# Optimization experiments

Measured on AMD Instinct MI355X. Metric: run time of the kernel, lower is better.

The kernel has to match this reference:

```python
import jax, jax.numpy as jnp
import numpy as np
from jax import lax

B, T = 8192, 4096


def setup_inputs() -> dict:
    key = jax.random.key(0)
    ks = jax.random.split(key, 16)
    P = jax.random.uniform(ks[0], (B, T, 1), dtype=jnp.float32) * 10.0  # precipitation, mm
    lengths = jax.random.randint(ks[1], (B,), 1, T + 1, dtype=jnp.int32)
    initial_S = jax.random.uniform(ks[2], (4,), dtype=jnp.float32) * 20.0  # initial tank levels
    Area = jnp.array([100.0], dtype=jnp.float32)  # catchment area km^2
    baseflow = jnp.array([0.0], dtype=jnp.float32)  # unused by forward, kept for signature fidelity

    def u(k, lo, hi):
        return jax.random.uniform(k, (1,), dtype=jnp.float32) * (hi - lo) + lo

    params = {
        "outflow_rate_1_h1": u(ks[3], 0.05, 0.25),
        "outflow_rate_1_h2": u(ks[4], 0.05, 0.10),
        "height_1_h1": u(ks[5], 40.0, 60.0),
        "height_1_h2": u(ks[6], 0.0, 40.0),
        "inflow_rate_2": u(ks[7], 0.01, 0.30),
        "outflow_rate_2": u(ks[8], 0.005, 0.30),
        "height_2": u(ks[9], 0.0, 30.0),
        "inflow_rate_3": u(ks[10], 0.005, 0.20),
        "outflow_rate_3": u(ks[11], 0.005, 0.15),
        "height_3": u(ks[12], 0.0, 30.0),
        "inflow_rate_4": u(ks[13], 0.005, 0.10),
        "outflow_rate_4": u(ks[14], 0.0006, 0.10),
    }
    return {"P": P, "lengths": lengths, "initial_S": initial_S, "Area": Area,
            "baseflow": baseflow, **params}


def reference(P, lengths, initial_S, Area, baseflow,
              outflow_rate_1_h1, outflow_rate_1_h2, height_1_h1, height_1_h2,
              inflow_rate_2, outflow_rate_2, height_2,
              inflow_rate_3, outflow_rate_3, height_3,
              inflow_rate_4, outflow_rate_4):
    Pq = P[..., 0]                              # [B, T]
    b, t = Pq.shape
    # valid_mask[b, t] = (lengths[b] > t), as in pad_packed_sequence masking
    mask = (jnp.arange(t)[None, :] < lengths[:, None]).astype(Pq.dtype)  # [B, T]
    w_init = tuple(jnp.broadcast_to(initial_S[i], (b,)) for i in range(4))

    def step(carry, xs):
        w1, w2, w3, w4 = carry
        p, m = xs                               # [B] each
        # Tank 1: two side outlets + bottom percolation into tank 2
        of1h1 = jnp.maximum(outflow_rate_1_h1 * (w1 - height_1_h1 + p), 0.0) * m
        of1h2 = jnp.maximum(outflow_rate_1_h2 * (w1 - height_1_h2 + p), 0.0) * m
        of1 = (of1h1 + of1h2) * m
        out12 = jnp.maximum(inflow_rate_2 * (w1 + p), 0.0) * m
        w1 = w1 + (p - of1 - out12) * m
        # Tank 2
        of2 = jnp.maximum(outflow_rate_2 * (w2 + out12 - height_2), 0.0) * m
        out23 = jnp.maximum(inflow_rate_3 * (w2 + out12), 0.0) * m
        w2 = w2 + (out12 - of2 - out23) * m
        # Tank 3
        of3 = jnp.maximum(outflow_rate_3 * (w3 + out23 - height_3), 0.0) * m
        out34 = jnp.maximum(inflow_rate_4 * (w3 + out23), 0.0) * m
        w3 = w3 + (out23 - of3 - out34) * m
        # Tank 4 (deep baseflow tank)
        of4 = jnp.maximum(outflow_rate_4 * (w4 + out34), 0.0) * m
        w4 = w4 + (out34 - of4) * m
        total = (of1 + of2 + of3 + of4) * m
        return (w1, w2, w3, w4), total * Area / 3.6   # mm -> m^3/s conversion

    _, ys = lax.scan(step, w_init, (Pq.T, mask.T))    # ys: [T, B]
    return ys.T                                        # [B, T]
```

## Files before the change

kernel.cpp:

```cpp
#include <hip/hip_runtime.h>
#include <stdint.h>


__device__ __forceinline__ float quad_rot1(float x) {
    int xi = __builtin_bit_cast(int, x);
    int r = __builtin_amdgcn_update_dpp(xi, xi, 0x93, 0xF, 0xF, false);
    return __builtin_bit_cast(float, r);
}

__device__ __forceinline__ float quad_bcast(float x, int s) {
    int xi = __builtin_bit_cast(int, x);
    int r;
    switch (s & 3) {
    case 0:  r = __builtin_amdgcn_update_dpp(xi, xi, 0x00, 0xF, 0xF, false); break;
    case 1:  r = __builtin_amdgcn_update_dpp(xi, xi, 0x55, 0xF, 0xF, false); break;
    case 2:  r = __builtin_amdgcn_update_dpp(xi, xi, 0xAA, 0xF, 0xF, false); break;
    default: r = __builtin_amdgcn_update_dpp(xi, xi, 0xFF, 0xF, 0xF, false); break;
    }
    return __builtin_bit_cast(float, r);
}

__global__ __launch_bounds__(64)
void tank_kernel(
    const float* __restrict__ P,
    const int*   __restrict__ lengths,
    const float* __restrict__ S0,
    const float* __restrict__ AreaP,
    const float* __restrict__ p_r1h1, const float* __restrict__ p_r1h2,
    const float* __restrict__ p_h1h1, const float* __restrict__ p_h1h2,
    const float* __restrict__ p_ri2,  const float* __restrict__ p_ro2,
    const float* __restrict__ p_h2,
    const float* __restrict__ p_ri3,  const float* __restrict__ p_ro3,
    const float* __restrict__ p_h3,
    const float* __restrict__ p_ri4,  const float* __restrict__ p_ro4,
    float* __restrict__ Out,
    int B, int T)
{
    __shared__ float4 outbuf[3 * 256];

    const int tid = threadIdx.x;
    const int g   = tid >> 2;
    const int k   = tid & 3;
    const int row = blockIdx.x * 16 + g;
    const int rowc = (row < B) ? row : (B - 1);
    const bool is0 = (k == 0);
    const bool is3 = (k == 3);
    const float zk = (k == 0) ? 0.0f : 1.0f;

    const float v_r1h1 = p_r1h1[0], v_r1h2 = p_r1h2[0];
    const float v_h11 = p_h1h1[0], v_h12 = p_h1h2[0];
    const float v_ri2 = p_ri2[0], v_ro2 = p_ro2[0], v_h2 = p_h2[0];
    const float v_ri3 = p_ri3[0], v_ro3 = p_ro3[0], v_h3 = p_h3[0];
    const float v_ri4 = p_ri4[0], v_ro4 = p_ro4[0];
    const float scale = AreaP[0] * (1.0f / 3.6f);

    float rA = v_ro4, kA = 0.0f, rB = 0.0f, kB = 0.0f, riN = 0.0f;
    if (k == 0) { rA = v_r1h1; kA = -v_r1h1 * v_h11; rB = v_r1h2; kB = -v_r1h2 * v_h12; riN = v_ri2; }
    else if (k == 1) { rA = v_ro2; kA = -v_ro2 * v_h2; riN = v_ri3; }
    else if (k == 2) { rA = v_ro3; kA = -v_ro3 * v_h3; riN = v_ri4; }

    float w = (k == 0) ? S0[0] : (k == 1) ? S0[1] : (k == 2) ? S0[2] : S0[3];

    int len = lengths[rowc];
    if (len > T) len = T;
    if (len < 0) len = 0;

    float fl0 = 0.0f, fl1 = 0.0f, fl2 = 0.0f, fl3 = 0.0f;
    float ps0 = 0.0f, ps1 = 0.0f, ps2 = 0.0f, ps3 = 0.0f;
    const int ntiles = T / 64;

#define HOP4(CX, CY, CZ, CW, FREEZE, hidx) do {                   \
        float r0_ = quad_rot1(fl0);                               \
        float r1_ = quad_rot1(fl1);                               \
        float r2_ = quad_rot1(fl2);                               \
        float r3_ = quad_rot1(fl3);                               \
        float q0_ = quad_rot1(ps0);                               \
        float q1_ = quad_rot1(ps1);                               \
        float q2_ = quad_rot1(ps2);                               \
        float q3_ = quad_rot1(ps3);                               \
        float i0_ = is0 ? (CX) : r0_;                             \
        float i1_ = is0 ? (CY) : r1_;                             \
        float i2_ = is0 ? (CZ) : r2_;                             \
        float i3_ = is0 ? (CW) : r3_;                             \
        float t_, a1_, a2_, e_, Y_, wn_;                          \
                                                      \
        t_  = w + i0_;                                            \
        a1_ = fmaxf(fmaf(rA, t_, kA), 0.0f);                      \
        a2_ = fmaxf(fmaf(rB, t_, kB), 0.0f);                      \
        e_  = fmaxf(t_, 0.0f);                                    \
        fl0 = riN * e_;                                           \
        Y_  = a1_ + a2_;                                          \
        wn_ = (t_ - fl0) - Y_;                                    \
        w = (FREEZE) ? (((hidx) >= k) ? wn_ : w) : wn_;           \
        ps0 = fmaf(q0_, zk, Y_);                                  \
                                                      \
        t_  = w + i1_;                                            \
        a1_ = fmaxf(fmaf(rA, t_, kA), 0.0f);                      \
        a2_ = fmaxf(fmaf(rB, t_, kB), 0.0f);                      \
        e_  = fmaxf(t_, 0.0f);                                    \
        fl1 = riN * e_;                                           \
        Y_  = a1_ + a2_;                                          \
        wn_ = (t_ - fl1) - Y_;                                    \
        w = (FREEZE) ? (((hidx) >= k) ? wn_ : w) : wn_;           \
        ps1 = fmaf(q1_, zk, Y_);                                  \
                                                      \
        t_  = w + i2_;                                            \
        a1_ = fmaxf(fmaf(rA, t_, kA), 0.0f);                      \
        a2_ = fmaxf(fmaf(rB, t_, kB), 0.0f);                      \
        e_  = fmaxf(t_, 0.0f);                                    \
        fl2 = riN * e_;                                           \
        Y_  = a1_ + a2_;                                          \
        wn_ = (t_ - fl2) - Y_;                                    \
        w = (FREEZE) ? (((hidx) >= k) ? wn_ : w) : wn_;           \
        ps2 = fmaf(q2_, zk, Y_);                                  \
                                                      \
        t_  = w + i3_;                                            \
        a1_ = fmaxf(fmaf(rA, t_, kA), 0.0f);                      \
        a2_ = fmaxf(fmaf(rB, t_, kB), 0.0f);                      \
        e_  = fmaxf(t_, 0.0f);                                    \
        fl3 = riN * e_;                                           \
        Y_  = a1_ + a2_;                                          \
        wn_ = (t_ - fl3) - Y_;                                    \
        w = (FREEZE) ? (((hidx) >= k) ? wn_ : w) : wn_;           \
        ps3 = fmaf(q3_, zk, Y_);                                  \
    } while (0)

#define STAGE_LOAD(stN, mt) do {                                          \
        const float* src_ = P + (size_t)rowc * T + (mt) * 64;             \
        _Pragma("unroll")                                                 \
        for (int r = 0; r < 4; ++r)                                       \
            stN[r] = *reinterpret_cast<const float4*>(src_ + (4 * r + k) * 4); \
    } while (0)

#define OUT_STORE(mt) do {                                                \
        const float4* ob_ = outbuf + ((mt) % 3) * 256;                    \
        const int col0_ = (mt) * 64;                                      \
        _Pragma("unroll")                                                 \
        for (int r = 0; r < 4; ++r) {                                     \
            float4 v_ = ob_[g * 16 + ((4 * r + k) ^ g)];                  \
            const int cb_ = col0_ + (4 * r + k) * 4;                      \
            float4 s_;                                                    \
            s_.x = (cb_ + 0 < len) ? v_.x * scale : 0.0f;                 \
            s_.y = (cb_ + 1 < len) ? v_.y * scale : 0.0f;                 \
            s_.z = (cb_ + 2 < len) ? v_.z * scale : 0.0f;                 \
            s_.w = (cb_ + 3 < len) ? v_.w * scale : 0.0f;                 \
            if (row < B)                                                  \
                *reinterpret_cast<float4*>(Out + (size_t)row * T + cb_) = s_; \
        }                                                                 \
    } while (0)

#define TILE_BODY(FREEZE, h0, stN) do {                                   \
        _Pragma("unroll")                                                 \
        for (int j4 = 0; j4 < 16; ++j4) {                                 \
            const float4 pv_ = stN[j4 >> 2];                              \
            float px_ = quad_bcast(pv_.x, j4);                            \
            float py_ = quad_bcast(pv_.y, j4);                            \
            float pz_ = quad_bcast(pv_.z, j4);                            \
            float pw_ = quad_bcast(pv_.w, j4);                            \
            HOP4(px_, py_, pz_, pw_, FREEZE, j4);                         \
            const int b_ = (h0) + j4 - 3;                                 \
            if ((!(FREEZE) || b_ >= 0) && is3) {                          \
                float4* obp_ = outbuf + ((b_ >> 4) % 3) * 256;            \
                obp_[g * 16 + ((b_ & 15) ^ g)] =                          \
                    make_float4(ps0, ps1, ps2, ps3);                      \
            }                                                             \
        }                                                                 \
    } while (0)

    float4 stA[4], stB[4];
    STAGE_LOAD(stA, 0);
    if (ntiles > 1) STAGE_LOAD(stB, 1);
    TILE_BODY(1, 0, stA);

    #pragma clang loop unroll(disable)
    for (int m = 1; m + 1 < ntiles; m += 2) {
        STAGE_LOAD(stA, m + 1);
        if (m >= 3) OUT_STORE(m - 2);
        TILE_BODY(0, m * 16, stB);
        STAGE_LOAD(stB, m + 2);
        OUT_STORE(m - 1);
        TILE_BODY(0, (m + 1) * 16, stA);
    }

    OUT_STORE(ntiles - 3);
    TILE_BODY(0, (ntiles - 1) * 16, stB);

    {
        const int nb = T >> 2;
        #pragma unroll
        for (int d = 0; d < 3; ++d) {
            HOP4(0.0f, 0.0f, 0.0f, 0.0f, 0, 0);
            const int b_ = nb - 3 + d;
            if (is3) {
                float4* obp = outbuf + ((b_ >> 4) % 3) * 256;
                obp[g * 16 + ((b_ & 15) ^ g)] = make_float4(ps0, ps1, ps2, ps3);
            }
        }
    }
#undef HOP4
#undef TILE_BODY

    OUT_STORE(ntiles - 2);
    OUT_STORE(ntiles - 1);
#undef OUT_STORE
#undef STAGE_LOAD
}

extern "C" void kernel_launch(void* const* d_in, const int* in_sizes, int n_in,
                              void* d_out, int out_size, void* d_ws, size_t ws_size,
                              hipStream_t stream) {
    const float* P        = (const float*)d_in[0];
    const int*   lengths  = (const int*)d_in[1];
    const float* S0       = (const float*)d_in[2];
    const float* Area     = (const float*)d_in[3];
    const float* r1h1 = (const float*)d_in[5];
    const float* r1h2 = (const float*)d_in[6];
    const float* h1h1 = (const float*)d_in[7];
    const float* h1h2 = (const float*)d_in[8];
    const float* ri2  = (const float*)d_in[9];
    const float* ro2  = (const float*)d_in[10];
    const float* h2   = (const float*)d_in[11];
    const float* ri3  = (const float*)d_in[12];
    const float* ro3  = (const float*)d_in[13];
    const float* h3   = (const float*)d_in[14];
    const float* ri4  = (const float*)d_in[15];
    const float* ro4  = (const float*)d_in[16];
    float* out = (float*)d_out;

    const int B = in_sizes[1];
    const int T = in_sizes[0] / B;

    dim3 block(64);
    dim3 grid((B + 15) / 16);
    hipLaunchKernelGGL(tank_kernel, grid, block, 0, stream,
                       P, lengths, S0, Area,
                       r1h1, r1h2, h1h1, h1h2,
                       ri2, ro2, h2, ri3, ro3, h3, ri4, ro4,
                       out, B, T);
}
```

Before: 379.4 us.

## Rewrite tank step as min of affine pieces to shorten the dependency chain

The per-step tank update (clamped outlet terms subtracted from level plus inflow) is rewritten as the minimum of four affine functions of the level w. All inflow-dependent terms are precomputed before the serial chain, so each step on the recurrence becomes four FMAs and a min-tree. The flow to the next tank becomes riN*w plus a precomputed term. This drops the max(t,0) clamp on percolation and so assumes the combined level stays nonnegative, which holds for nonnegative precipitation and initial levels.

```diff
diff --git a/kernel.cpp b/kernel.cpp
--- a/kernel.cpp
+++ b/kernel.cpp
@@ -54,10 +54,18 @@
     const float v_ri4 = p_ri4[0], v_ro4 = p_ro4[0];
     const float scale = AreaP[0] * (1.0f / 3.6f);
 
-    float rA = v_ro4, kA = 0.0f, rB = 0.0f, kB = 0.0f, riN = 0.0f;
-    if (k == 0) { rA = v_r1h1; kA = -v_r1h1 * v_h11; rB = v_r1h2; kB = -v_r1h2 * v_h12; riN = v_ri2; }
-    else if (k == 1) { rA = v_ro2; kA = -v_ro2 * v_h2; riN = v_ri3; }
-    else if (k == 2) { rA = v_ro3; kA = -v_ro3 * v_h3; riN = v_ri4; }
+    float rA = v_ro4, hA = 0.0f, rB = 0.0f, hB = 0.0f, riN = 0.0f;
+    if (k == 0) { rA = v_r1h1; hA = v_h11; rB = v_r1h2; hB = v_h12; riN = v_ri2; }
+    else if (k == 1) { rA = v_ro2; hA = v_h2; riN = v_ri3; }
+    else if (k == 2) { rA = v_ro3; hA = v_h3; riN = v_ri4; }
+
+    const float s0c = 1.0f - riN;
+    const float s1c = s0c - rA;
+    const float s2c = s0c - rB;
+    const float s3c = s1c - rB;
+    const float c1c = rA * hA;
+    const float c2c = rB * hB;
+    const float c3c = c1c + c2c;
 
     float w = (k == 0) ? S0[0] : (k == 1) ? S0[1] : (k == 2) ? S0[2] : S0[3];
 
@@ -69,60 +77,55 @@
     float ps0 = 0.0f, ps1 = 0.0f, ps2 = 0.0f, ps3 = 0.0f;
     const int ntiles = T / 64;
 
-#define HOP4(CX, CY, CZ, CW, FREEZE, hidx) do {                   \
-        float r0_ = quad_rot1(fl0);                               \
-        float r1_ = quad_rot1(fl1);                               \
-        float r2_ = quad_rot1(fl2);                               \
-        float r3_ = quad_rot1(fl3);                               \
-        float q0_ = quad_rot1(ps0);                               \
-        float q1_ = quad_rot1(ps1);                               \
-        float q2_ = quad_rot1(ps2);                               \
-        float q3_ = quad_rot1(ps3);                               \
-        float i0_ = is0 ? (CX) : r0_;                             \
-        float i1_ = is0 ? (CY) : r1_;                             \
-        float i2_ = is0 ? (CZ) : r2_;                             \
-        float i3_ = is0 ? (CW) : r3_;                             \
-        float t_, a1_, a2_, e_, Y_, wn_;                          \
-                                                      \
-        t_  = w + i0_;                                            \
-        a1_ = fmaxf(fmaf(rA, t_, kA), 0.0f);                      \
-        a2_ = fmaxf(fmaf(rB, t_, kB), 0.0f);                      \
-        e_  = fmaxf(t_, 0.0f);                                    \
-        fl0 = riN * e_;                                           \
-        Y_  = a1_ + a2_;                                          \
-        wn_ = (t_ - fl0) - Y_;                                    \
-        w = (FREEZE) ? (((hidx) >= k) ? wn_ : w) : wn_;           \
-        ps0 = fmaf(q0_, zk, Y_);                                  \
-                                                      \
-        t_  = w + i1_;                                            \
-        a1_ = fmaxf(fmaf(rA, t_, kA), 0.0f);                      \
-        a2_ = fmaxf(fmaf(rB, t_, kB), 0.0f);                      \
-        e_  = fmaxf(t_, 0.0f);                                    \
-        fl1 = riN * e_;                                           \
-        Y_  = a1_ + a2_;                                          \
-        wn_ = (t_ - fl1) - Y_;                                    \
-        w = (FREEZE) ? (((hidx) >= k) ? wn_ : w) : wn_;           \
-        ps1 = fmaf(q1_, zk, Y_);                                  \
-                                                      \
-        t_  = w + i2_;                                            \
-        a1_ = fmaxf(fmaf(rA, t_, kA), 0.0f);                      \
-        a2_ = fmaxf(fmaf(rB, t_, kB), 0.0f);                      \
-        e_  = fmaxf(t_, 0.0f);                                    \
-        fl2 = riN * e_;                                           \
-        Y_  = a1_ + a2_;                                          \
-        wn_ = (t_ - fl2) - Y_;                                    \
-        w = (FREEZE) ? (((hidx) >= k) ? wn_ : w) : wn_;           \
-        ps2 = fmaf(q2_, zk, Y_);                                  \
-                                                      \
-        t_  = w + i3_;                                            \
-        a1_ = fmaxf(fmaf(rA, t_, kA), 0.0f);                      \
-        a2_ = fmaxf(fmaf(rB, t_, kB), 0.0f);                      \
-        e_  = fmaxf(t_, 0.0f);                                    \
-        fl3 = riN * e_;                                           \
-        Y_  = a1_ + a2_;                                          \
-        wn_ = (t_ - fl3) - Y_;                                    \
-        w = (FREEZE) ? (((hidx) >= k) ? wn_ : w) : wn_;           \
-        ps3 = fmaf(q3_, zk, Y_);                                  \
+#define STEP1(E0, E1, E2, E3, FF, QQ, FLOUT, PSOUT, FREEZE, hidx) do {  \
+        float l0_ = fmaf(s0c, w, E0);                                   \
+        float l1_ = fmaf(s1c, w, E1);                                   \
+        float l2_ = fmaf(s2c, w, E2);                                   \
+        float l3_ = fmaf(s3c, w, E3);                                   \
+        float wn_ = fminf(fminf(l0_, l1_), fminf(l2_, l3_));            \
+        FLOUT = fmaf(riN, w, FF);                                       \
+        float Y_ = l0_ - wn_;                                           \
+        w = (FREEZE) ? (((hidx) >= k) ? wn_ : w) : wn_;                 \
+        PSOUT = fmaf(QQ, zk, Y_);                                       \
+    } while (0)
+
+#define HOP4(CX, CY, CZ, CW, FREEZE, hidx) do {                         \
+        float r0_ = quad_rot1(fl0);                                     \
+        float r1_ = quad_rot1(fl1);                                     \
+        float r2_ = quad_rot1(fl2);                                     \
+        float r3_ = quad_rot1(fl3);                                     \
+        float q0_ = quad_rot1(ps0);                                     \
+        float q1_ = quad_rot1(ps1);                                     \
+        float q2_ = quad_rot1(ps2);                                     \
+        float q3_ = quad_rot1(ps3);                                     \
+        float i0_ = is0 ? (CX) : r0_;                                   \
+        float i1_ = is0 ? (CY) : r1_;                                   \
+        float i2_ = is0 ? (CZ) : r2_;                                   \
+        float i3_ = is0 ? (CW) : r3_;                                   \
+        float e00_ = s0c * i0_;                                         \
+        float e01_ = fmaf(s1c, i0_, c1c);                               \
+        float e02_ = fmaf(s2c, i0_, c2c);                               \
+        float e03_ = fmaf(s3c, i0_, c3c);                               \
+        float f0_  = riN * i0_;                                         \
+        float e10_ = s0c * i1_;                                         \
+        float e11_ = fmaf(s1c, i1_, c1c);                               \
+        float e12_ = fmaf(s2c, i1_, c2c);                               \
+        float e13_ = fmaf(s3c, i1_, c3c);                               \
+        float f1_  = riN * i1_;                                         \
+        float e20_ = s0c * i2_;                                         \
+        float e21_ = fmaf(s1c, i2_, c1c);                               \
+        float e22_ = fmaf(s2c, i2_, c2c);                               \
+        float e23_ = fmaf(s3c, i2_, c3c);                               \
+        float f2_  = riN * i2_;                                         \
+        float e30_ = s0c * i3_;                                         \
+        float e31_ = fmaf(s1c, i3_, c1c);                               \
+        float e32_ = fmaf(s2c, i3_, c2c);                               \
+        float e33_ = fmaf(s3c, i3_, c3c);                               \
+        float f3_  = riN * i3_;                                         \
+        STEP1(e00_, e01_, e02_, e03_, f0_, q0_, fl0, ps0, FREEZE, hidx);\
+        STEP1(e10_, e11_, e12_, e13_, f1_, q1_, fl1, ps1, FREEZE, hidx);\
+        STEP1(e20_, e21_, e22_, e23_, f2_, q2_, fl2, ps2, FREEZE, hidx);\
+        STEP1(e30_, e31_, e32_, e33_, f3_, q3_, fl3, ps3, FREEZE, hidx);\
     } while (0)
 
 #define STAGE_LOAD(stN, mt) do {                                          \
@@ -198,6 +201,7 @@
         }
     }
 #undef HOP4
+#undef STEP1
 #undef TILE_BODY
 
     OUT_STORE(ntiles - 2);
```

Measured after the change: 394.6 us. 1.04x slower.
